# Kernel optimization log

Hardware: AMD Instinct MI355X
Metric: run time of the kernel (lower is better)

The kernel has to match this reference:

```python
import jax, jax.numpy as jnp
import numpy as np
from jax import lax

B, CHI, CHO, H, W = 8, 128, 128, 64, 64
K = 3
KK = K * K


def setup_inputs() -> dict:
    key = jax.random.key(0)
    ks = jax.random.split(key, 7)
    x = jax.random.normal(ks[0], (B, CHI, H, W), jnp.float32)
    # small offset-conv weights so sampled offsets stay in a realistic few-pixel range
    off_w = jax.random.normal(ks[1], (3 * KK, CHI, K, K), jnp.float32) * 0.01
    off_b = jnp.zeros((3 * KK,), jnp.float32)
    w = jax.random.normal(ks[2], (CHO, CHI, K, K), jnp.float32) / np.sqrt(CHI * KK).astype(np.float32)
    b = jnp.zeros((CHO,), jnp.float32)
    gamma = jax.random.uniform(ks[3], (CHO,), jnp.float32)  # nn.init.uniform_ on BN weight
    beta = jnp.zeros((CHO,), jnp.float32)
    return {"x": x, "off_w": off_w, "off_b": off_b, "w": w, "b": b, "gamma": gamma, "beta": beta}


def _deform_conv(x, off_w, off_b, w, b):
    """DCNv2 modulated deformable conv, k=3, stride=1, pad=1, dil=1, 1 deform group."""
    B_, C, H_, W_ = x.shape
    # offset/mask branch: plain 3x3 conv -> 27 channels (2*9 offsets, 9 masks)
    om = lax.conv_general_dilated(x, off_w, (1, 1), ((1, 1), (1, 1)),
                                  dimension_numbers=("NCHW", "OIHW", "NCHW"))
    om = om + off_b[None, :, None, None]
    off = om[:, : 2 * KK].reshape(B_, KK, 2, H_, W_)  # [B,9,2,H,W]; ch 2k=y, 2k+1=x
    mask = jax.nn.sigmoid(om[:, 2 * KK:])             # [B,9,H,W]

    ky, kx = jnp.meshgrid(jnp.arange(K, dtype=jnp.float32),
                          jnp.arange(K, dtype=jnp.float32), indexing="ij")
    ky = ky.reshape(KK); kx = kx.reshape(KK)
    # sampling positions: p = p0 - pad + k*dil + offset
    py = off[:, :, 0] + (jnp.arange(H_, dtype=jnp.float32) - 1.0)[None, None, :, None] + ky[None, :, None, None]
    px = off[:, :, 1] + (jnp.arange(W_, dtype=jnp.float32) - 1.0)[None, None, None, :] + kx[None, :, None, None]

    y0 = jnp.floor(py); x0 = jnp.floor(px)
    ly = py - y0; lx = px - x0
    xf = x.reshape(B_, C, H_ * W_)

    def corner(yi, xi, wgt):
        valid = ((yi >= 0) & (yi <= H_ - 1) & (xi >= 0) & (xi <= W_ - 1)).astype(x.dtype)
        yc = jnp.clip(yi, 0, H_ - 1).astype(jnp.int32)
        xc = jnp.clip(xi, 0, W_ - 1).astype(jnp.int32)
        idx = (yc * W_ + xc).reshape(B_, KK * H_ * W_)
        g = jax.vmap(lambda xb, ib: xb[:, ib])(xf, idx).reshape(B_, C, KK, H_, W_)
        return g * (valid * wgt)[:, None]

    val = (corner(y0, x0, (1 - ly) * (1 - lx))
           + corner(y0, x0 + 1, (1 - ly) * lx)
           + corner(y0 + 1, x0, ly * (1 - lx))
           + corner(y0 + 1, x0 + 1, ly * lx))  # [B,C,9,H,W]
    val = val * mask[:, None]  # modulation
    out = jnp.einsum("bckhw,ock->bohw", val, w.reshape(w.shape[0], C, KK))
    return out + b[None, :, None, None]


def reference(x, off_w, off_b, w, b, gamma, beta):
    y = _deform_conv(x, off_w, off_b, w, b)
    # BatchNorm2d in training mode (batch statistics), eps=1e-5, then ReLU
    mean = y.mean(axis=(0, 2, 3))
    var = y.var(axis=(0, 2, 3))
    yn = (y - mean[None, :, None, None]) * lax.rsqrt(var[None, :, None, None] + 1e-5)
    return jax.nn.relu(yn * gamma[None, :, None, None] + beta[None, :, None, None])
```

## Files before the change

### kernel.cpp

```cpp
#include <hip/hip_runtime.h>
#include <hip/hip_bf16.h>
#include <math.h>

#define HH 64
#define WW 64
#define HW 4096
#define LDV 136
#define NSLOT 16

typedef __bf16 bf16x8 __attribute__((ext_vector_type(8)));
typedef float floatx4 __attribute__((ext_vector_type(4)));
typedef unsigned int uint4a __attribute__((ext_vector_type(4)));
typedef unsigned int uint2a __attribute__((ext_vector_type(2)));

#define WS_Y    0u
#define WS_XTB  16777216u
#define WS_WTB  25165824u
#define WS_OWB  25460736u
#define WS_PSQ  25534464u

static __device__ inline ushort f2bf(float f) {
  __hip_bfloat16 h = __float2bfloat16(f);
  return __builtin_bit_cast(ushort, h);
}
static __device__ inline float lo16(unsigned int u) { return __builtin_bit_cast(float, u << 16); }
static __device__ inline float hi16(unsigned int u) { return __builtin_bit_cast(float, u & 0xffff0000u); }

__global__ __launch_bounds__(256) void k_prep(const float* __restrict__ x,
                                              const float* __restrict__ w,
                                              const float* __restrict__ ow,
                                              ushort* __restrict__ xtb,
                                              ushort* __restrict__ wtb,
                                              ushort* __restrict__ owb,
                                              float* __restrict__ psq) {
  __shared__ float tile[32][33];
  int bid = blockIdx.x;
  if (bid < 4096) {
    int hw0 = (bid & 127) * 32;
    int c0 = ((bid >> 7) & 3) * 32;
    int b = bid >> 9;
    int col = threadIdx.x & 31, row = threadIdx.x >> 5;
    const float* xb = x + ((size_t)b * 128 + c0) * HW + hw0;
#pragma unroll
    for (int i = 0; i < 32; i += 8)
      tile[row + i][col] = xb[(size_t)(row + i) * HW + col];
    __syncthreads();
    int hw = threadIdx.x >> 3, cq = threadIdx.x & 7;
    ushort* xo = xtb + ((size_t)b * HW + hw0) * 128 + c0;
    unsigned int lo = (unsigned int)f2bf(tile[cq * 4 + 0][hw]) |
                      ((unsigned int)f2bf(tile[cq * 4 + 1][hw]) << 16);
    unsigned int hi = (unsigned int)f2bf(tile[cq * 4 + 2][hw]) |
                      ((unsigned int)f2bf(tile[cq * 4 + 3][hw]) << 16);
    uint2a v2 = (uint2a){lo, hi};
    *(uint2a*)(&xo[(size_t)hw * 128 + cq * 4]) = v2;
  } else if (bid < 4096 + 576) {
    int idx = (bid - 4096) * 256 + threadIdx.x;
    int c = idx & 127, o = (idx >> 7) & 127, k = idx >> 14;
    wtb[idx] = f2bf(w[(o * 128 + c) * 9 + k]);
  } else if (bid < 4096 + 720) {
    int j = (bid - 4672) * 256 + threadIdx.x;
    int c = j & 127, o = (j >> 7) & 31, k = j >> 12;
    float v = (o < 27) ? ow[(o * 128 + c) * 9 + k] : 0.f;
    owb[j] = f2bf(v);
  } else {
    for (int i = threadIdx.x; i < NSLOT * 256; i += 256) psq[i] = 0.f;
  }
}

__global__ __launch_bounds__(256) void k_main(
    const ushort* __restrict__ xtb, const ushort* __restrict__ wtb,
    const ushort* __restrict__ owb, const float* __restrict__ off_b,
    const float* __restrict__ bias, float* __restrict__ y,
    float* __restrict__ psq) {
  __shared__ ushort Vl[2][32 * LDV];
  __shared__ float omL[27 * 32];
  int t = threadIdx.x;
  int lane = t & 63, wv = t >> 6;
  int li = lane & 15, quad = lane >> 4;
  int bid = blockIdx.x;
  int b = bid & 7;
  int hr = bid >> 3;
  int row = hr >> 1, p0b = (hr & 1) * 32;
  const ushort* xb = xtb + (size_t)b * HW * 128;
  int ch = t & 15;
  int pq = t >> 4;

  int mi = wv & 1, ni = wv >> 1;
  floatx4 oacc = (floatx4){0.f, 0.f, 0.f, 0.f};
  uint4a u0, u1;
  auto p1load = [&](int k, int p, uint4a& u) {
    int ky = k / 3, kx = k % 3;
    int ry = row - 1 + ky, cx = p0b + p - 1 + kx;
    bool v = (ry >= 0 && ry < HH && cx >= 0 && cx < WW);
    int idx = v ? (ry * WW + cx) : 0;
    uint4a a = *(const uint4a*)(xb + (size_t)idx * 128 + ch * 8);
    u = v ? a : (uint4a){0u, 0u, 0u, 0u};
  };
  p1load(0, pq, u0);
  p1load(0, pq + 16, u1);
  for (int k = 0; k < 9; ++k) {
    *(uint4a*)(&Vl[k & 1][pq * LDV + ch * 8]) = u0;
    *(uint4a*)(&Vl[k & 1][(pq + 16) * LDV + ch * 8]) = u1;
    if (k < 8) {
      p1load(k + 1, pq, u0);
      p1load(k + 1, pq + 16, u1);
    }
    __syncthreads();
#pragma unroll
    for (int ks = 0; ks < 4; ++ks) {
      bf16x8 bfrag = __builtin_bit_cast(bf16x8,
          *(const uint4a*)(&Vl[k & 1][(ni * 16 + li) * LDV + ks * 32 + quad * 8]));
      bf16x8 afrag = __builtin_bit_cast(bf16x8,
          *(const uint4a*)(&owb[(size_t)(k * 32 + mi * 16 + li) * 128 + ks * 32 + quad * 8]));
      oacc = __builtin_amdgcn_mfma_f32_16x16x32_bf16(afrag, bfrag, oacc, 0, 0, 0);
    }
  }
#pragma unroll
  for (int r = 0; r < 4; ++r) {
    int o = mi * 16 + quad * 4 + r;
    if (o < 27) omL[o * 32 + ni * 16 + li] = oacc[r] + off_b[o];
  }
  __syncthreads();

  floatx4 macc[2][2];
#pragma unroll
  for (int i = 0; i < 2; ++i)
#pragma unroll
    for (int j = 0; j < 2; ++j) macc[i][j] = (floatx4){0.f, 0.f, 0.f, 0.f};

  float wqA[4], wqB[4];
  int idxA[4], idxB[4];
  uint4a u[8];

  auto prep = [&](int k, int p, float* wq, int* idx4) {
    int ky = k / 3, kx = k % 3;
    float offy = omL[(2 * k) * 32 + p];
    float offx = omL[(2 * k + 1) * 32 + p];
    float mraw = omL[(18 + k) * 32 + p];
    float m = 1.f / (1.f + __expf(-mraw));
    float py = offy + (float)(row - 1 + ky);
    float px = offx + (float)(p0b + p - 1 + kx);
    float y0f = floorf(py), x0f = floorf(px);
    float ly = py - y0f, lx = px - x0f;
    int iy0 = (int)y0f, ix0 = (int)x0f;
    int iy1 = iy0 + 1, ix1 = ix0 + 1;
    float w00 = (1.f - ly) * (1.f - lx) * m, w01 = (1.f - ly) * lx * m;
    float w10 = ly * (1.f - lx) * m, w11 = ly * lx * m;
    if (iy0 < 0 || iy0 > HH - 1) { w00 = 0.f; w01 = 0.f; }
    if (iy1 < 0 || iy1 > HH - 1) { w10 = 0.f; w11 = 0.f; }
    if (ix0 < 0 || ix0 > WW - 1) { w00 = 0.f; w10 = 0.f; }
    if (ix1 < 0 || ix1 > WW - 1) { w01 = 0.f; w11 = 0.f; }
    int cy0 = min(max(iy0, 0), HH - 1), cy1 = min(max(iy1, 0), HH - 1);
    int cx0 = min(max(ix0, 0), WW - 1), cx1 = min(max(ix1, 0), WW - 1);
    idx4[0] = cy0 * WW + cx0;
    idx4[1] = cy0 * WW + cx1;
    idx4[2] = cy1 * WW + cx0;
    idx4[3] = cy1 * WW + cx1;
    wq[0] = w00; wq[1] = w01; wq[2] = w10; wq[3] = w11;
  };
  auto issue = [&]() {
#pragma unroll
    for (int c = 0; c < 4; ++c)
      u[c] = *(const uint4a*)(xb + (size_t)idxA[c] * 128 + ch * 8);
#pragma unroll
    for (int c = 0; c < 4; ++c)
      u[4 + c] = *(const uint4a*)(xb + (size_t)idxB[c] * 128 + ch * 8);
  };

  prep(0, pq, wqA, idxA);
  prep(0, pq + 16, wqB, idxB);
  issue();
  for (int k = 0; k < 9; ++k) {
    {
      uint4a outv;
#pragma unroll
      for (int e = 0; e < 4; ++e) {
        float rlo = wqA[0] * lo16(u[0][e]) + wqA[1] * lo16(u[1][e]) +
                    wqA[2] * lo16(u[2][e]) + wqA[3] * lo16(u[3][e]);
        float rhi = wqA[0] * hi16(u[0][e]) + wqA[1] * hi16(u[1][e]) +
                    wqA[2] * hi16(u[2][e]) + wqA[3] * hi16(u[3][e]);
        outv[e] = (unsigned int)f2bf(rlo) | ((unsigned int)f2bf(rhi) << 16);
      }
      *(uint4a*)(&Vl[k & 1][pq * LDV + ch * 8]) = outv;
    }
    {
      uint4a outv;
#pragma unroll
      for (int e = 0; e < 4; ++e) {
        float rlo = wqB[0] * lo16(u[4][e]) + wqB[1] * lo16(u[5][e]) +
                    wqB[2] * lo16(u[6][e]) + wqB[3] * lo16(u[7][e]);
        float rhi = wqB[0] * hi16(u[4][e]) + wqB[1] * hi16(u[5][e]) +
                    wqB[2] * hi16(u[6][e]) + wqB[3] * hi16(u[7][e]);
        outv[e] = (unsigned int)f2bf(rlo) | ((unsigned int)f2bf(rhi) << 16);
      }
      *(uint4a*)(&Vl[k & 1][(pq + 16) * LDV + ch * 8]) = outv;
    }
    if (k < 8) {
      prep(k + 1, pq, wqA, idxA);
      prep(k + 1, pq + 16, wqB, idxB);
      issue();
    }
    __syncthreads();
    const ushort* Arow = &wtb[(size_t)(k * 128 + wv * 32) * 128];
#pragma unroll
    for (int ks = 0; ks < 4; ++ks) {
      bf16x8 b0 = __builtin_bit_cast(bf16x8,
          *(const uint4a*)(&Vl[k & 1][(li)*LDV + ks * 32 + quad * 8]));
      bf16x8 b1 = __builtin_bit_cast(bf16x8,
          *(const uint4a*)(&Vl[k & 1][(16 + li) * LDV + ks * 32 + quad * 8]));
      bf16x8 a0 = __builtin_bit_cast(bf16x8,
          *(const uint4a*)(Arow + (size_t)(li)*128 + ks * 32 + quad * 8));
      bf16x8 a1 = __builtin_bit_cast(bf16x8,
          *(const uint4a*)(Arow + (size_t)(16 + li) * 128 + ks * 32 + quad * 8));
      macc[0][0] = __builtin_amdgcn_mfma_f32_16x16x32_bf16(a0, b0, macc[0][0], 0, 0, 0);
      macc[0][1] = __builtin_amdgcn_mfma_f32_16x16x32_bf16(a0, b1, macc[0][1], 0, 0, 0);
      macc[1][0] = __builtin_amdgcn_mfma_f32_16x16x32_bf16(a1, b0, macc[1][0], 0, 0, 0);
      macc[1][1] = __builtin_amdgcn_mfma_f32_16x16x32_bf16(a1, b1, macc[1][1], 0, 0, 0);
    }
  }

  int slot = bid & (NSLOT - 1);
#pragma unroll
  for (int ot = 0; ot < 2; ++ot)
#pragma unroll
    for (int r = 0; r < 4; ++r) {
      int o = wv * 32 + ot * 16 + quad * 4 + r;
      float v0 = macc[ot][0][r] + bias[o];
      float v1 = macc[ot][1][r] + bias[o];
      y[((size_t)(b * 128 + o)) * HW + row * 64 + p0b + li] = v0;
      y[((size_t)(b * 128 + o)) * HW + row * 64 + p0b + 16 + li] = v1;
      float s = v0 + v1, q = v0 * v0 + v1 * v1;
#pragma unroll
      for (int m = 1; m < 16; m <<= 1) {
        s += __shfl_xor(s, m, 64);
        q += __shfl_xor(q, m, 64);
      }
      if (li == 0) {
        atomicAdd(&psq[slot * 256 + o], s);
        atomicAdd(&psq[slot * 256 + 128 + o], q);
      }
    }
}

__global__ __launch_bounds__(256) void k_norm(const float* __restrict__ y,
                                              const float* __restrict__ psq,
                                              const float* __restrict__ gamma,
                                              const float* __restrict__ beta,
                                              float* __restrict__ out) {
  int blk = blockIdx.x;
  int b = blk & 7;
  int o = (blk >> 3) & 127;
  int qseg = blk >> 10;
  float s = 0.f, q = 0.f;
#pragma unroll
  for (int j = 0; j < NSLOT; ++j) {
    s += psq[j * 256 + o];
    q += psq[j * 256 + 128 + o];
  }
  float mean = s * (1.f / 32768.f);
  float var = q * (1.f / 32768.f) - mean * mean;
  float scale = gamma[o] * rsqrtf(var + 1e-5f);
  float shift = beta[o] - mean * scale;
  int i4 = (b * 128 + o) * 1024 + qseg * 256 + threadIdx.x;
  float4 v = ((const float4*)y)[i4];
  float4 r;
  r.x = fmaxf(v.x * scale + shift, 0.f);
  r.y = fmaxf(v.y * scale + shift, 0.f);
  r.z = fmaxf(v.z * scale + shift, 0.f);
  r.w = fmaxf(v.w * scale + shift, 0.f);
  ((float4*)out)[i4] = r;
}

extern "C" void kernel_launch(void* const* d_in, const int* in_sizes, int n_in,
                              void* d_out, int out_size, void* d_ws, size_t ws_size,
                              hipStream_t stream) {
  const float* x     = (const float*)d_in[0];
  const float* off_w = (const float*)d_in[1];
  const float* off_b = (const float*)d_in[2];
  const float* w     = (const float*)d_in[3];
  const float* bias  = (const float*)d_in[4];
  const float* gamma = (const float*)d_in[5];
  const float* beta  = (const float*)d_in[6];
  float* out = (float*)d_out;
  char* ws = (char*)d_ws;

  float* y    = (float*)(ws + WS_Y);
  ushort* xtb = (ushort*)(ws + WS_XTB);
  ushort* wtb = (ushort*)(ws + WS_WTB);
  ushort* owb = (ushort*)(ws + WS_OWB);
  float* psq  = (float*)(ws + WS_PSQ);

  k_prep<<<4817, 256, 0, stream>>>(x, w, off_w, xtb, wtb, owb, psq);
  k_main<<<1024, 256, 0, stream>>>(xtb, wtb, owb, off_b, bias, y, psq);
  k_norm<<<4096, 256, 0, stream>>>(y, psq, gamma, beta, out);
}
```

Before: 158.0 us.

## Warp-specialize main kernel into producer gather waves and consumer MFMA waves

Doubles the block to 512 threads and splits it into four producer waves, which do the bilinear gather/interpolation and write the LDS tiles, and four consumer waves, which run the MFMA over them. Each stage runs one step ahead of the other, so gather latency can overlap with the matrix multiplies. The cost is a barrier per step shared by 8 waves, a tighter register budget from launch_bounds(512,4), and producer waves sitting idle during the epilogue.

```diff
diff --git a/kernel.cpp b/kernel.cpp
--- a/kernel.cpp
+++ b/kernel.cpp
@@ -67,7 +67,7 @@
   }
 }
 
-__global__ __launch_bounds__(256) void k_main(
+__global__ __launch_bounds__(512, 4) void k_main(
     const ushort* __restrict__ xtb, const ushort* __restrict__ wtb,
     const ushort* __restrict__ owb, const float* __restrict__ off_b,
     const float* __restrict__ bias, float* __restrict__ y,
@@ -76,18 +76,20 @@
   __shared__ float omL[27 * 32];
   int t = threadIdx.x;
   int lane = t & 63, wv = t >> 6;
-  int li = lane & 15, quad = lane >> 4;
+  bool isProd = (wv < 4);
+  int cwv = wv - 4;
+  int li = lane & 15, quad = (lane >> 4) & 3;
   int bid = blockIdx.x;
   int b = bid & 7;
   int hr = bid >> 3;
   int row = hr >> 1, p0b = (hr & 1) * 32;
   const ushort* xb = xtb + (size_t)b * HW * 128;
   int ch = t & 15;
-  int pq = t >> 4;
-
-  int mi = wv & 1, ni = wv >> 1;
+  int pq = (t >> 4) & 15;
+
+  int mi = cwv & 1, ni = cwv >> 1;
   floatx4 oacc = (floatx4){0.f, 0.f, 0.f, 0.f};
-  uint4a u0, u1;
+  uint4a uA0, uB0, uA1, uB1;
   auto p1load = [&](int k, int p, uint4a& u) {
     int ky = k / 3, kx = k % 3;
     int ry = row - 1 + ky, cx = p0b + p - 1 + kx;
@@ -96,41 +98,73 @@
     uint4a a = *(const uint4a*)(xb + (size_t)idx * 128 + ch * 8);
     u = v ? a : (uint4a){0u, 0u, 0u, 0u};
   };
-  p1load(0, pq, u0);
-  p1load(0, pq + 16, u1);
-  for (int k = 0; k < 9; ++k) {
-    *(uint4a*)(&Vl[k & 1][pq * LDV + ch * 8]) = u0;
-    *(uint4a*)(&Vl[k & 1][(pq + 16) * LDV + ch * 8]) = u1;
-    if (k < 8) {
-      p1load(k + 1, pq, u0);
-      p1load(k + 1, pq + 16, u1);
-    }
-    __syncthreads();
+  auto p1mfma = [&](int k, int buf) {
 #pragma unroll
     for (int ks = 0; ks < 4; ++ks) {
       bf16x8 bfrag = __builtin_bit_cast(bf16x8,
-          *(const uint4a*)(&Vl[k & 1][(ni * 16 + li) * LDV + ks * 32 + quad * 8]));
+          *(const uint4a*)(&Vl[buf][(ni * 16 + li) * LDV + ks * 32 + quad * 8]));
       bf16x8 afrag = __builtin_bit_cast(bf16x8,
           *(const uint4a*)(&owb[(size_t)(k * 32 + mi * 16 + li) * 128 + ks * 32 + quad * 8]));
       oacc = __builtin_amdgcn_mfma_f32_16x16x32_bf16(afrag, bfrag, oacc, 0, 0, 0);
     }
-  }
-#pragma unroll
-  for (int r = 0; r < 4; ++r) {
-    int o = mi * 16 + quad * 4 + r;
-    if (o < 27) omL[o * 32 + ni * 16 + li] = oacc[r] + off_b[o];
+  };
+
+  if (isProd) {
+    p1load(0, pq, uA0);
+    p1load(0, pq + 16, uB0);
+    *(uint4a*)(&Vl[0][pq * LDV + ch * 8]) = uA0;
+    *(uint4a*)(&Vl[0][(pq + 16) * LDV + ch * 8]) = uB0;
+    p1load(1, pq, uA1);
+    p1load(1, pq + 16, uB1);
   }
   __syncthreads();
 
+#define P1STEP(K, UWA, UWB, ULA, ULB)                                         \
+  do {                                                                        \
+    if (isProd) {                                                             \
+      if ((K) < 8) {                                                          \
+        *(uint4a*)(&Vl[((K) + 1) & 1][pq * LDV + ch * 8]) = UWA;              \
+        *(uint4a*)(&Vl[((K) + 1) & 1][(pq + 16) * LDV + ch * 8]) = UWB;       \
+        if ((K) < 7) {                                                        \
+          p1load((K) + 2, pq, ULA);                                           \
+          p1load((K) + 2, pq + 16, ULB);                                      \
+        }                                                                     \
+      }                                                                       \
+    } else {                                                                  \
+      p1mfma((K), (K) & 1);                                                   \
+    }                                                                         \
+    __syncthreads();                                                          \
+  } while (0)
+
+  P1STEP(0, uA1, uB1, uA0, uB0);
+  P1STEP(1, uA0, uB0, uA1, uB1);
+  P1STEP(2, uA1, uB1, uA0, uB0);
+  P1STEP(3, uA0, uB0, uA1, uB1);
+  P1STEP(4, uA1, uB1, uA0, uB0);
+  P1STEP(5, uA0, uB0, uA1, uB1);
+  P1STEP(6, uA1, uB1, uA0, uB0);
+  P1STEP(7, uA0, uB0, uA1, uB1);
+  P1STEP(8, uA1, uB1, uA0, uB0);
+#undef P1STEP
+
+  if (!isProd) {
+#pragma unroll
+    for (int r = 0; r < 4; ++r) {
+      int o = mi * 16 + quad * 4 + r;
+      if (o < 27) omL[o * 32 + ni * 16 + li] = oacc[r] + off_b[o];
+    }
+  }
+  __syncthreads();
+
   floatx4 macc[2][2];
 #pragma unroll
   for (int i = 0; i < 2; ++i)
 #pragma unroll
     for (int j = 0; j < 2; ++j) macc[i][j] = (floatx4){0.f, 0.f, 0.f, 0.f};
 
-  float wqA[4], wqB[4];
+  float wqA0[4], wqB0[4], wqA1[4], wqB1[4];
   int idxA[4], idxB[4];
-  uint4a u[8];
+  uint4a U[8];
 
   auto prep = [&](int k, int p, float* wq, int* idx4) {
     int ky = k / 3, kx = k % 3;
@@ -161,53 +195,19 @@
   auto issue = [&]() {
 #pragma unroll
     for (int c = 0; c < 4; ++c)
-      u[c] = *(const uint4a*)(xb + (size_t)idxA[c] * 128 + ch * 8);
+      U[c] = *(const uint4a*)(xb + (size_t)idxA[c] * 128 + ch * 8);
 #pragma unroll
     for (int c = 0; c < 4; ++c)
-      u[4 + c] = *(const uint4a*)(xb + (size_t)idxB[c] * 128 + ch * 8);
-  };
-
-  prep(0, pq, wqA, idxA);
-  prep(0, pq + 16, wqB, idxB);
-  issue();
-  for (int k = 0; k < 9; ++k) {
-    {
-      uint4a outv;
-#pragma unroll
-      for (int e = 0; e < 4; ++e) {
-        float rlo = wqA[0] * lo16(u[0][e]) + wqA[1] * lo16(u[1][e]) +
-                    wqA[2] * lo16(u[2][e]) + wqA[3] * lo16(u[3][e]);
-        float rhi = wqA[0] * hi16(u[0][e]) + wqA[1] * hi16(u[1][e]) +
-                    wqA[2] * hi16(u[2][e]) + wqA[3] * hi16(u[3][e]);
-        outv[e] = (unsigned int)f2bf(rlo) | ((unsigned int)f2bf(rhi) << 16);
-      }
-      *(uint4a*)(&Vl[k & 1][pq * LDV + ch * 8]) = outv;
-    }
-    {
-      uint4a outv;
-#pragma unroll
-      for (int e = 0; e < 4; ++e) {
-        float rlo = wqB[0] * lo16(u[4][e]) + wqB[1] * lo16(u[5][e]) +
-                    wqB[2] * lo16(u[6][e]) + wqB[3] * lo16(u[7][e]);
-        float rhi = wqB[0] * hi16(u[4][e]) + wqB[1] * hi16(u[5][e]) +
-                    wqB[2] * hi16(u[6][e]) + wqB[3] * hi16(u[7][e]);
-        outv[e] = (unsigned int)f2bf(rlo) | ((unsigned int)f2bf(rhi) << 16);
-      }
-      *(uint4a*)(&Vl[k & 1][(pq + 16) * LDV + ch * 8]) = outv;
-    }
-    if (k < 8) {
-      prep(k + 1, pq, wqA, idxA);
-      prep(k + 1, pq + 16, wqB, idxB);
-      issue();
-    }
-    __syncthreads();
-    const ushort* Arow = &wtb[(size_t)(k * 128 + wv * 32) * 128];
+      U[4 + c] = *(const uint4a*)(xb + (size_t)idxB[c] * 128 + ch * 8);
+  };
+  auto p2mfma = [&](int k, int buf) {
+    const ushort* Arow = &wtb[(size_t)(k * 128 + cwv * 32) * 128];
 #pragma unroll
     for (int ks = 0; ks < 4; ++ks) {
       bf16x8 b0 = __builtin_bit_cast(bf16x8,
-          *(const uint4a*)(&Vl[k & 1][(li)*LDV + ks * 32 + quad * 8]));
+          *(const uint4a*)(&Vl[buf][(li)*LDV + ks * 32 + quad * 8]));
       bf16x8 b1 = __builtin_bit_cast(bf16x8,
-          *(const uint4a*)(&Vl[k & 1][(16 + li) * LDV + ks * 32 + quad * 8]));
+          *(const uint4a*)(&Vl[buf][(16 + li) * LDV + ks * 32 + quad * 8]));
       bf16x8 a0 = __builtin_bit_cast(bf16x8,
           *(const uint4a*)(Arow + (size_t)(li)*128 + ks * 32 + quad * 8));
       bf16x8 a1 = __builtin_bit_cast(bf16x8,
@@ -217,29 +217,87 @@
       macc[1][0] = __builtin_amdgcn_mfma_f32_16x16x32_bf16(a1, b0, macc[1][0], 0, 0, 0);
       macc[1][1] = __builtin_amdgcn_mfma_f32_16x16x32_bf16(a1, b1, macc[1][1], 0, 0, 0);
     }
-  }
-
-  int slot = bid & (NSLOT - 1);
-#pragma unroll
-  for (int ot = 0; ot < 2; ++ot)
-#pragma unroll
-    for (int r = 0; r < 4; ++r) {
-      int o = wv * 32 + ot * 16 + quad * 4 + r;
-      float v0 = macc[ot][0][r] + bias[o];
-      float v1 = macc[ot][1][r] + bias[o];
-      y[((size_t)(b * 128 + o)) * HW + row * 64 + p0b + li] = v0;
-      y[((size_t)(b * 128 + o)) * HW + row * 64 + p0b + 16 + li] = v1;
-      float s = v0 + v1, q = v0 * v0 + v1 * v1;
-#pragma unroll
-      for (int m = 1; m < 16; m <<= 1) {
-        s += __shfl_xor(s, m, 64);
-        q += __shfl_xor(q, m, 64);
+  };
+
+#define CONVW(UP, WQ, ROWP, BUF)                                              \
+  do {                                                                        \
+    uint4a outv;                                                              \
+    _Pragma("unroll")                                                         \
+    for (int e = 0; e < 4; ++e) {                                             \
+      float rlo = WQ[0] * lo16((UP)[0][e]) + WQ[1] * lo16((UP)[1][e]) +       \
+                  WQ[2] * lo16((UP)[2][e]) + WQ[3] * lo16((UP)[3][e]);        \
+      float rhi = WQ[0] * hi16((UP)[0][e]) + WQ[1] * hi16((UP)[1][e]) +       \
+                  WQ[2] * hi16((UP)[2][e]) + WQ[3] * hi16((UP)[3][e]);        \
+      outv[e] = (unsigned int)f2bf(rlo) | ((unsigned int)f2bf(rhi) << 16);    \
+    }                                                                         \
+    *(uint4a*)(&Vl[BUF][(ROWP)*LDV + ch * 8]) = outv;                         \
+  } while (0)
+
+  if (isProd) {
+    prep(0, pq, wqA0, idxA);
+    prep(0, pq + 16, wqB0, idxB);
+    issue();
+    CONVW(U, wqA0, pq, 0);
+    CONVW((U + 4), wqB0, pq + 16, 0);
+    prep(1, pq, wqA1, idxA);
+    prep(1, pq + 16, wqB1, idxB);
+    issue();
+  }
+  __syncthreads();
+
+#define P2STEP(K, WQAW, WQBW, WQAL, WQBL)                                     \
+  do {                                                                        \
+    if (isProd) {                                                             \
+      if ((K) < 8) {                                                          \
+        CONVW(U, WQAW, pq, ((K) + 1) & 1);                                    \
+        CONVW((U + 4), WQBW, pq + 16, ((K) + 1) & 1);                         \
+        if ((K) < 7) {                                                        \
+          prep((K) + 2, pq, WQAL, idxA);                                      \
+          prep((K) + 2, pq + 16, WQBL, idxB);                                 \
+          issue();                                                            \
+        }                                                                     \
+      }                                                                       \
+    } else {                                                                  \
+      p2mfma((K), (K) & 1);                                                   \
+    }                                                                         \
+    __syncthreads();                                                          \
+  } while (0)
+
+  P2STEP(0, wqA1, wqB1, wqA0, wqB0);
+  P2STEP(1, wqA0, wqB0, wqA1, wqB1);
+  P2STEP(2, wqA1, wqB1, wqA0, wqB0);
+  P2STEP(3, wqA0, wqB0, wqA1, wqB1);
+  P2STEP(4, wqA1, wqB1, wqA0, wqB0);
+  P2STEP(5, wqA0, wqB0, wqA1, wqB1);
+  P2STEP(6, wqA1, wqB1, wqA0, wqB0);
+  P2STEP(7, wqA0, wqB0, wqA1, wqB1);
+  P2STEP(8, wqA1, wqB1, wqA0, wqB0);
+#undef P2STEP
+#undef CONVW
+
+  if (!isProd) {
+    int slot = bid & (NSLOT - 1);
+#pragma unroll
+    for (int ot = 0; ot < 2; ++ot)
+#pragma unroll
+      for (int r = 0; r < 4; ++r) {
+        int o = cwv * 32 + ot * 16 + quad * 4 + r;
+        float v0 = macc[ot][0][r] + bias[o];
+        float v1 = macc[ot][1][r] + bias[o];
+        y[((size_t)(b * 128 + o)) * HW + row * 64 + p0b + li] = v0;
+        y[((size_t)(b * 128 + o)) * HW + row * 64 + p0b + 16 + li] = v1;
+        float s = v0 + v1, q = v0 * v0 + v1 * v1;
+#pragma unroll
+        for (int m = 1; m < 16; m <<= 1) {
+          s += __shfl_xor(s, m, 64);
+          q += __shfl_xor(q, m, 64);
+        }
+        if (li == 0) {
+          atomicAdd(&psq[slot * 256 + o], s);
+          atomicAdd(&psq[slot * 256 + 128 + o], q);
+        }
       }
-      if (li == 0) {
-        atomicAdd(&psq[slot * 256 + o], s);
-        atomicAdd(&psq[slot * 256 + 128 + o], q);
-      }
-    }
+  }
 }
 
 __global__ __launch_bounds__(256) void k_norm(const float* __restrict__ y,
@@ -291,6 +349,6 @@
   float* psq  = (float*)(ws + WS_PSQ);
 
   k_prep<<<4817, 256, 0, stream>>>(x, w, off_w, xtb, wtb, owb, psq);
-  k_main<<<1024, 256, 0, stream>>>(xtb, wtb, owb, off_b, bias, y, psq);
+  k_main<<<1024, 512, 0, stream>>>(xtb, wtb, owb, off_b, bias, y, psq);
   k_norm<<<4096, 256, 0, stream>>>(y, psq, gamma, beta, out);
 }
```

Result: slower. 163.3 us (+3.4%).

## Split offset-conv into separate kernel with row-tile LDS staging

Applied to the files above, without the earlier changes.

Moves the 27-channel offset/mask conv out of the main deformable kernel into a dedicated kernel that stages three full input rows in LDS and computes a 64-pixel row per block, writing offsets to a workspace buffer. The deform kernel then just loads precomputed offsets. This removes the per-k global reload and sync loop from the main kernel, and the LDS staging reuses each input pixel across the three kx taps. The cost is an extra launch plus a global round trip for the offset tensor.

```diff
diff --git a/kernel.cpp b/kernel.cpp
--- a/kernel.cpp
+++ b/kernel.cpp
@@ -18,6 +18,7 @@
 #define WS_WTB  25165824u
 #define WS_OWB  25460736u
 #define WS_PSQ  25534464u
+#define WS_OM   25550848u
 
 static __device__ inline ushort f2bf(float f) {
   __hip_bfloat16 h = __float2bfloat16(f);
@@ -67,11 +68,69 @@
   }
 }
 
-__global__ __launch_bounds__(256) void k_main(
+__global__ __launch_bounds__(256) void k_off(const ushort* __restrict__ xtb,
+                                             const ushort* __restrict__ owb,
+                                             const float* __restrict__ off_b,
+                                             float* __restrict__ om) {
+  __shared__ ushort S[3 * 64 * LDV];
+  int t = threadIdx.x;
+  int lane = t & 63, wv = t >> 6;
+  int li = lane & 15, quad = (lane >> 4) & 3;
+  int bid = blockIdx.x;
+  int b = bid & 7;
+  int row = bid >> 3;
+  const ushort* xb = xtb + (size_t)b * HW * 128;
+
+#pragma unroll
+  for (int i = 0; i < 12; ++i) {
+    int idx = t + i * 256;
+    int rr = idx >> 10;
+    int rem = idx & 1023;
+    int col = rem >> 4, chunk = rem & 15;
+    int gy = row - 1 + rr;
+    uint4a v = (uint4a){0u, 0u, 0u, 0u};
+    if (gy >= 0 && gy < HH)
+      v = *(const uint4a*)(xb + ((size_t)(gy * WW + col)) * 128 + chunk * 8);
+    *(uint4a*)(&S[(rr * 64 + col) * LDV + chunk * 8]) = v;
+  }
+  __syncthreads();
+
+  int pxbase = wv * 16;
+  floatx4 acc0 = (floatx4){0.f, 0.f, 0.f, 0.f};
+  floatx4 acc1 = (floatx4){0.f, 0.f, 0.f, 0.f};
+  for (int k = 0; k < 9; ++k) {
+    int ky = k / 3, kx = k % 3;
+    int c = pxbase + li - 1 + kx;
+    bool ok = (c >= 0 && c < WW);
+    int cc = min(max(c, 0), WW - 1);
+#pragma unroll
+    for (int ks = 0; ks < 4; ++ks) {
+      uint4a bv = *(const uint4a*)(&S[(ky * 64 + cc) * LDV + ks * 32 + quad * 8]);
+      bv = ok ? bv : (uint4a){0u, 0u, 0u, 0u};
+      bf16x8 bf = __builtin_bit_cast(bf16x8, bv);
+      bf16x8 a0 = __builtin_bit_cast(bf16x8,
+          *(const uint4a*)(&owb[(size_t)(k * 32 + li) * 128 + ks * 32 + quad * 8]));
+      bf16x8 a1 = __builtin_bit_cast(bf16x8,
+          *(const uint4a*)(&owb[(size_t)(k * 32 + 16 + li) * 128 + ks * 32 + quad * 8]));
+      acc0 = __builtin_amdgcn_mfma_f32_16x16x32_bf16(a0, bf, acc0, 0, 0, 0);
+      acc1 = __builtin_amdgcn_mfma_f32_16x16x32_bf16(a1, bf, acc1, 0, 0, 0);
+    }
+  }
+  int px = row * WW + pxbase + li;
+#pragma unroll
+  for (int r = 0; r < 4; ++r) {
+    int o0 = quad * 4 + r;
+    om[((size_t)b * 27 + o0) * HW + px] = acc0[r] + off_b[o0];
+    int o1 = 16 + quad * 4 + r;
+    if (o1 < 27)
+      om[((size_t)b * 27 + o1) * HW + px] = acc1[r] + off_b[o1];
+  }
+}
+
+__global__ __launch_bounds__(256) void k_deform(
     const ushort* __restrict__ xtb, const ushort* __restrict__ wtb,
-    const ushort* __restrict__ owb, const float* __restrict__ off_b,
-    const float* __restrict__ bias, float* __restrict__ y,
-    float* __restrict__ psq) {
+    const float* __restrict__ om, const float* __restrict__ bias,
+    float* __restrict__ y, float* __restrict__ psq) {
   __shared__ ushort Vl[2][32 * LDV];
   __shared__ float omL[27 * 32];
   int t = threadIdx.x;
@@ -85,40 +144,9 @@
   int ch = t & 15;
   int pq = t >> 4;
 
-  int mi = wv & 1, ni = wv >> 1;
-  floatx4 oacc = (floatx4){0.f, 0.f, 0.f, 0.f};
-  uint4a u0, u1;
-  auto p1load = [&](int k, int p, uint4a& u) {
-    int ky = k / 3, kx = k % 3;
-    int ry = row - 1 + ky, cx = p0b + p - 1 + kx;
-    bool v = (ry >= 0 && ry < HH && cx >= 0 && cx < WW);
-    int idx = v ? (ry * WW + cx) : 0;
-    uint4a a = *(const uint4a*)(xb + (size_t)idx * 128 + ch * 8);
-    u = v ? a : (uint4a){0u, 0u, 0u, 0u};
-  };
-  p1load(0, pq, u0);
-  p1load(0, pq + 16, u1);
-  for (int k = 0; k < 9; ++k) {
-    *(uint4a*)(&Vl[k & 1][pq * LDV + ch * 8]) = u0;
-    *(uint4a*)(&Vl[k & 1][(pq + 16) * LDV + ch * 8]) = u1;
-    if (k < 8) {
-      p1load(k + 1, pq, u0);
-      p1load(k + 1, pq + 16, u1);
-    }
-    __syncthreads();
-#pragma unroll
-    for (int ks = 0; ks < 4; ++ks) {
-      bf16x8 bfrag = __builtin_bit_cast(bf16x8,
-          *(const uint4a*)(&Vl[k & 1][(ni * 16 + li) * LDV + ks * 32 + quad * 8]));
-      bf16x8 afrag = __builtin_bit_cast(bf16x8,
-          *(const uint4a*)(&owb[(size_t)(k * 32 + mi * 16 + li) * 128 + ks * 32 + quad * 8]));
-      oacc = __builtin_amdgcn_mfma_f32_16x16x32_bf16(afrag, bfrag, oacc, 0, 0, 0);
-    }
-  }
-#pragma unroll
-  for (int r = 0; r < 4; ++r) {
-    int o = mi * 16 + quad * 4 + r;
-    if (o < 27) omL[o * 32 + ni * 16 + li] = oacc[r] + off_b[o];
+  for (int i = t; i < 27 * 32; i += 256) {
+    int o = i >> 5, p = i & 31;
+    omL[o * 32 + p] = om[((size_t)b * 27 + o) * HW + row * 64 + p0b + p];
   }
   __syncthreads();
 
@@ -289,8 +317,10 @@
   ushort* wtb = (ushort*)(ws + WS_WTB);
   ushort* owb = (ushort*)(ws + WS_OWB);
   float* psq  = (float*)(ws + WS_PSQ);
+  float* om   = (float*)(ws + WS_OM);
 
   k_prep<<<4817, 256, 0, stream>>>(x, w, off_w, xtb, wtb, owb, psq);
-  k_main<<<1024, 256, 0, stream>>>(xtb, wtb, owb, off_b, bias, y, psq);
+  k_off<<<512, 256, 0, stream>>>(xtb, owb, off_b, om);
+  k_deform<<<1024, 256, 0, stream>>>(xtb, wtb, om, bias, y, psq);
   k_norm<<<4096, 256, 0, stream>>>(y, psq, gamma, beta, out);
 }
```

Measured after the change: 161.8 us. 1.02x slower.
